# Performance work log

Measured on AMD Instinct MI355X. Metric: run time of the kernel, lower is better.

Reference implementation:

```python
import jax, jax.numpy as jnp
import numpy as np

M, K, N = 131072, 512, 512


def setup_inputs() -> dict:
    key = jax.random.key(0)
    k1, k2, k3, k4 = jax.random.split(key, 4)
    # Simulated int8 quantized values held in float32 (real kernel uses int8)
    x = jnp.round(jax.random.normal(k1, (M, K), dtype=jnp.float32) * 30.0)
    weight = jnp.round(jax.random.normal(k2, (N, K), dtype=jnp.float32) * 30.0)
    # per-token activation scale [M,1], per-output-channel weight scale [N]
    x_scale = jax.random.uniform(k3, (M, 1), dtype=jnp.float32, minval=1e-3, maxval=2e-2)
    weight_scale = jax.random.uniform(k4, (N,), dtype=jnp.float32, minval=1e-3, maxval=2e-2)
    return {"x": x, "x_scale": x_scale, "weight": weight, "weight_scale": weight_scale}


def reference(x, x_scale, weight, weight_scale):
    # gemm_a8w8(per_Token): out[m,n] = (sum_k x[m,k]*W[n,k]) * x_scale[m] * w_scale[n]
    acc = jnp.einsum('mk,nk->mn', x, weight)          # [M, N] int32-equivalent accum
    out = acc * x_scale * weight_scale[None, :]       # fused dequant scaling
    return out  # otype would be bf16 in the original; kept fp32 as reference baseline
```

## Files before the change

kernel.cpp:

```cpp
#include <hip/hip_runtime.h>
#include <hip/hip_bf16.h>
#include <stdint.h>

#define K_DIM 512
#define N_DIM 512
#define BM 64
#define CHUNK_K 64
#define CHUNK_FLOATS (BM * CHUNK_K)

typedef __bf16 bf16x8 __attribute__((ext_vector_type(8)));
typedef float floatx4 __attribute__((ext_vector_type(4)));

__device__ __forceinline__ bf16x8 cvt8(float4 a, float4 b) {
    bf16x8 r;
    r[0] = (__bf16)a.x; r[1] = (__bf16)a.y; r[2] = (__bf16)a.z; r[3] = (__bf16)a.w;
    r[4] = (__bf16)b.x; r[5] = (__bf16)b.y; r[6] = (__bf16)b.z; r[7] = (__bf16)b.w;
    return r;
}

__global__ __launch_bounds__(512) void wconv_kernel(const float* __restrict__ w,
                                                    __bf16* __restrict__ wf) {
    int t = blockIdx.x * 512 + threadIdx.x;
    int lane = t & 63, slot = t >> 6;
    int n = ((slot >> 4) << 4) + (lane & 15);
    int k = ((slot & 15) << 5) + ((lane >> 4) << 3);
    const float* src = w + (size_t)n * K_DIM + k;
    float4 f0 = *(const float4*)src;
    float4 f1 = *(const float4*)(src + 4);
    *(bf16x8*)(wf + (size_t)t * 8) = cvt8(f0, f1);
}

__device__ __forceinline__ void stage_chunk(const float* __restrict__ x,
                                            int rowBase, int kBase,
                                            float* ldsBuf, int wid, int lane) {
    #pragma unroll
    for (int i = 0; i < 2; ++i) {
        int sl = i * 8 + wid;
        int row = sl * 4 + (lane >> 4);
        int srcByte = ((lane & 15) << 4) ^ ((row & 7) << 4);
        const float* g = x + (size_t)(rowBase + row) * K_DIM + kBase + (srcByte >> 2);
        float* l = ldsBuf + sl * 1024 / 4;
        __builtin_amdgcn_global_load_lds(
            (const __attribute__((address_space(1))) void*)g,
            (__attribute__((address_space(3))) void*)l, 16, 0, 0);
    }
}

__device__ __forceinline__ bf16x8 read_afrag(const float* ldsBuf, int mg, int rt,
                                             int kcl, int lane) {
    int row = mg * 32 + rt * 16 + (lane & 15);
    int sw = (row & 7) << 4;
    int b0 = kcl * 128 + ((lane >> 4) << 5);
    const char* rb = (const char*)(ldsBuf + row * CHUNK_K);
    float4 fa = *(const float4*)(rb + (b0 ^ sw));
    float4 fb = *(const float4*)(rb + ((b0 + 16) ^ sw));
    return cvt8(fa, fb);
}

template <bool USE_WF>
__global__ __launch_bounds__(512, 2) void gemm_kernel(
    const float* __restrict__ x, const float* __restrict__ xscale,
    const __bf16* __restrict__ wf, const float* __restrict__ w,
    const float* __restrict__ wscale, float* __restrict__ out,
    int ntiles, int tilesPerBlock)
{
    __shared__ float lds[2 * CHUNK_FLOATS];
    const int t = threadIdx.x;
    const int lane = t & 63;
    const int wid = t >> 6;
    const int mg = wid >> 2;
    const int ng = wid & 3;
    const int laneR = lane & 15;

    const int tile0 = blockIdx.x * tilesPerBlock;
    if (tile0 >= ntiles) return;
    const int tileEnd = (tile0 + tilesPerBlock < ntiles) ? (tile0 + tilesPerBlock) : ntiles;
    const int nChunks = (tileEnd - tile0) * 8;

    floatx4 acc[2][8];
    bf16x8 wfr[8][2];

    stage_chunk(x, tile0 * BM, 0, &lds[0], wid, lane);

    for (int c = 0; c < nChunks; ++c) {
        const int tile = tile0 + (c >> 3);
        const int kk = c & 7;

        if (c > 0)
            asm volatile("s_waitcnt lgkmcnt(0)\n\ts_barrier" ::: "memory");

        #pragma unroll
        for (int nt = 0; nt < 8; ++nt) {
            int ntg = ng * 8 + nt;
            #pragma unroll
            for (int kcl = 0; kcl < 2; ++kcl) {
                int kcg = kk * 2 + kcl;
                if (USE_WF) {
                    wfr[nt][kcl] = *(const bf16x8*)(wf + (size_t)(((ntg << 4) + kcg) * 64 + lane) * 8);
                } else {
                    int n = (ntg << 4) + laneR;
                    const float* src = w + (size_t)n * K_DIM + (kcg << 5) + ((lane >> 4) << 3);
                    wfr[nt][kcl] = cvt8(*(const float4*)src, *(const float4*)(src + 4));
                }
            }
        }
        __builtin_amdgcn_sched_barrier(0);

        if (c + 1 < nChunks) {
            int cn = c + 1;
            stage_chunk(x, (tile0 + (cn >> 3)) * BM, (cn & 7) * CHUNK_K,
                        &lds[(cn & 1) * CHUNK_FLOATS], wid, lane);
            __builtin_amdgcn_sched_barrier(0);
            asm volatile("s_waitcnt vmcnt(2)\n\ts_barrier" ::: "memory");
        } else {
            asm volatile("s_waitcnt vmcnt(0)\n\ts_barrier" ::: "memory");
        }

        if (kk == 0) {
            #pragma unroll
            for (int i = 0; i < 2; ++i)
                #pragma unroll
                for (int j = 0; j < 8; ++j) acc[i][j] = (floatx4)0.f;
        }

        const float* cb = &lds[(c & 1) * CHUNK_FLOATS];
        #pragma unroll
        for (int kcl = 0; kcl < 2; ++kcl) {
            bf16x8 ax[2];
            #pragma unroll
            for (int rt = 0; rt < 2; ++rt)
                ax[rt] = read_afrag(cb, mg, rt, kcl, lane);
            #pragma unroll
            for (int nt = 0; nt < 8; ++nt)
                #pragma unroll
                for (int rt = 0; rt < 2; ++rt)
                    acc[rt][nt] = __builtin_amdgcn_mfma_f32_16x16x32_bf16(
                        wfr[nt][kcl], ax[rt], acc[rt][nt], 0, 0, 0);
        }

        if (kk == 7) {
            const int rowb = tile * BM;
            #pragma unroll
            for (int rt = 0; rt < 2; ++rt) {
                int m = rowb + mg * 32 + rt * 16 + laneR;
                float xs = xscale[m];
                #pragma unroll
                for (int nt = 0; nt < 8; ++nt) {
                    int nb = ng * 128 + (nt << 4) + ((lane >> 4) << 2);
                    float4 wsc = *(const float4*)(wscale + nb);
                    floatx4 a = acc[rt][nt];
                    float4 o;
                    o.x = a[0] * xs * wsc.x;
                    o.y = a[1] * xs * wsc.y;
                    o.z = a[2] * xs * wsc.z;
                    o.w = a[3] * xs * wsc.w;
                    *(float4*)(out + (size_t)m * N_DIM + nb) = o;
                }
            }
        }
    }
}

extern "C" void kernel_launch(void* const* d_in, const int* in_sizes, int n_in,
                              void* d_out, int out_size, void* d_ws, size_t ws_size,
                              hipStream_t stream) {
    const float* x      = (const float*)d_in[0];
    const float* xscale = (const float*)d_in[1];
    const float* w      = (const float*)d_in[2];
    const float* wscale = (const float*)d_in[3];
    float* out          = (float*)d_out;

    const int M = in_sizes[0] / K_DIM;
    const int ntiles = M / BM;
    const int nblocks = (ntiles < 256) ? ntiles : 256;
    const int tpb = (ntiles + nblocks - 1) / nblocks;

    if (ws_size >= (size_t)(N_DIM * K_DIM * sizeof(unsigned short))) {
        __bf16* wfp = (__bf16*)d_ws;
        wconv_kernel<<<dim3(64), dim3(512), 0, stream>>>(w, wfp);
        gemm_kernel<true><<<dim3(nblocks), dim3(512), 0, stream>>>(
            x, xscale, wfp, w, wscale, out, ntiles, tpb);
    } else {
        gemm_kernel<false><<<dim3(nblocks), dim3(512), 0, stream>>>(
            x, xscale, nullptr, w, wscale, out, ntiles, tpb);
    }
}
```

Measured before the change: 233.4 us.

## Use 1024-thread blocks with triple-buffered LDS and prefetched weight fragments

Doubles the block to 16 waves so each wave owns a 64-wide N slice, which halves the per-wave accumulators and weight fragments. The x staging ring grows from two to three LDS buffers and is issued two chunks ahead, and the next chunk's weight fragments are loaded into a second register set while the current chunk computes. The goal is to hide global load latency behind the MFMA work. In exchange there are more waves per block synchronising at each barrier, and the hand-tuned vmcnt counts must exactly match the number of outstanding loads.

```diff
diff --git a/kernel.cpp b/kernel.cpp
--- a/kernel.cpp
+++ b/kernel.cpp
@@ -7,6 +7,7 @@
 #define BM 64
 #define CHUNK_K 64
 #define CHUNK_FLOATS (BM * CHUNK_K)
+#define NBUF 3
 
 typedef __bf16 bf16x8 __attribute__((ext_vector_type(8)));
 typedef float floatx4 __attribute__((ext_vector_type(4)));
@@ -33,17 +34,13 @@
 __device__ __forceinline__ void stage_chunk(const float* __restrict__ x,
                                             int rowBase, int kBase,
                                             float* ldsBuf, int wid, int lane) {
-    #pragma unroll
-    for (int i = 0; i < 2; ++i) {
-        int sl = i * 8 + wid;
-        int row = sl * 4 + (lane >> 4);
-        int srcByte = ((lane & 15) << 4) ^ ((row & 7) << 4);
-        const float* g = x + (size_t)(rowBase + row) * K_DIM + kBase + (srcByte >> 2);
-        float* l = ldsBuf + sl * 1024 / 4;
-        __builtin_amdgcn_global_load_lds(
-            (const __attribute__((address_space(1))) void*)g,
-            (__attribute__((address_space(3))) void*)l, 16, 0, 0);
-    }
+    int row = wid * 4 + (lane >> 4);
+    int srcByte = ((lane & 15) << 4) ^ ((row & 7) << 4);
+    const float* g = x + (size_t)(rowBase + row) * K_DIM + kBase + (srcByte >> 2);
+    float* l = ldsBuf + wid * 256;
+    __builtin_amdgcn_global_load_lds(
+        (const __attribute__((address_space(1))) void*)g,
+        (__attribute__((address_space(3))) void*)l, 16, 0, 0);
 }
 
 __device__ __forceinline__ bf16x8 read_afrag(const float* ldsBuf, int mg, int rt,
@@ -58,106 +55,141 @@
 }
 
 template <bool USE_WF>
-__global__ __launch_bounds__(512, 2) void gemm_kernel(
+__device__ __forceinline__ void load_wfrag(bf16x8 (&dst)[4][2], int c,
+                                           const __bf16* __restrict__ wf,
+                                           const float* __restrict__ w,
+                                           int ng, int lane) {
+    int kk = c & 7;
+    #pragma unroll
+    for (int nt = 0; nt < 4; ++nt) {
+        int ntg = ng * 4 + nt;
+        #pragma unroll
+        for (int kcl = 0; kcl < 2; ++kcl) {
+            int kcg = kk * 2 + kcl;
+            if (USE_WF) {
+                dst[nt][kcl] = *(const bf16x8*)(wf + (size_t)(((ntg << 4) + kcg) * 64 + lane) * 8);
+            } else {
+                int n = (ntg << 4) + (lane & 15);
+                const float* s = w + (size_t)n * K_DIM + (kcg << 5) + ((lane >> 4) << 3);
+                dst[nt][kcl] = cvt8(*(const float4*)s, *(const float4*)(s + 4));
+            }
+        }
+    }
+}
+
+template <bool USE_WF>
+__device__ __forceinline__ void chunk_body(
+    int c, int nChunks, int ibR, int tile0,
+    const float* __restrict__ x, const float* __restrict__ xscale,
+    const __bf16* __restrict__ wf, const float* __restrict__ w,
+    const float* __restrict__ wscale, float* __restrict__ out,
+    float* lds, bf16x8 (&wfU)[4][2], bf16x8 (&wfF)[4][2], floatx4 (&acc)[2][4],
+    int wid, int lane, int mg, int ng)
+{
+    constexpr int WOPS = USE_WF ? 8 : 16;
+    const int laneR = lane & 15;
+
+    asm volatile("s_waitcnt lgkmcnt(0)\n\ts_barrier" ::: "memory");
+
+    {
+        int cn = (c + 1 < nChunks) ? c + 1 : nChunks - 1;
+        load_wfrag<USE_WF>(wfF, cn, wf, w, ng, lane);
+    }
+    __builtin_amdgcn_sched_barrier(0);
+
+    {
+        int cs = (c + 2 < nChunks) ? c + 2 : nChunks - 1;
+        int ibS = ibR + 2; if (ibS >= NBUF) ibS -= NBUF;
+        stage_chunk(x, (tile0 + (cs >> 3)) * BM, (cs & 7) * CHUNK_K,
+                    lds + ibS * CHUNK_FLOATS, wid, lane);
+    }
+    __builtin_amdgcn_sched_barrier(0);
+
+    if (c > 0 && (c & 7) == 0)
+        asm volatile("s_waitcnt vmcnt(%0)\n\ts_barrier" :: "i"(WOPS + 12) : "memory");
+    else
+        asm volatile("s_waitcnt vmcnt(%0)\n\ts_barrier" :: "i"(WOPS + 2) : "memory");
+
+    if ((c & 7) == 0) {
+        #pragma unroll
+        for (int i = 0; i < 2; ++i)
+            #pragma unroll
+            for (int j = 0; j < 4; ++j) acc[i][j] = (floatx4)0.f;
+    }
+
+    const float* cb = lds + ibR * CHUNK_FLOATS;
+    #pragma unroll
+    for (int kcl = 0; kcl < 2; ++kcl) {
+        bf16x8 ax[2];
+        #pragma unroll
+        for (int rt = 0; rt < 2; ++rt)
+            ax[rt] = read_afrag(cb, mg, rt, kcl, lane);
+        #pragma unroll
+        for (int nt = 0; nt < 4; ++nt)
+            #pragma unroll
+            for (int rt = 0; rt < 2; ++rt)
+                acc[rt][nt] = __builtin_amdgcn_mfma_f32_16x16x32_bf16(
+                    wfU[nt][kcl], ax[rt], acc[rt][nt], 0, 0, 0);
+    }
+
+    if ((c & 7) == 7) {
+        const int rowb = (tile0 + (c >> 3)) * BM;
+        #pragma unroll
+        for (int rt = 0; rt < 2; ++rt) {
+            int m = rowb + mg * 32 + rt * 16 + laneR;
+            float xs = xscale[m];
+            #pragma unroll
+            for (int nt = 0; nt < 4; ++nt) {
+                int nb = ng * 64 + (nt << 4) + ((lane >> 4) << 2);
+                float4 wsc = *(const float4*)(wscale + nb);
+                floatx4 a = acc[rt][nt];
+                float4 o;
+                o.x = a[0] * xs * wsc.x;
+                o.y = a[1] * xs * wsc.y;
+                o.z = a[2] * xs * wsc.z;
+                o.w = a[3] * xs * wsc.w;
+                *(float4*)(out + (size_t)m * N_DIM + nb) = o;
+            }
+        }
+    }
+}
+
+template <bool USE_WF>
+__global__ __launch_bounds__(1024) void gemm_kernel(
     const float* __restrict__ x, const float* __restrict__ xscale,
     const __bf16* __restrict__ wf, const float* __restrict__ w,
     const float* __restrict__ wscale, float* __restrict__ out,
     int ntiles, int tilesPerBlock)
 {
-    __shared__ float lds[2 * CHUNK_FLOATS];
+    __shared__ __align__(16) float lds[NBUF * CHUNK_FLOATS];
     const int t = threadIdx.x;
     const int lane = t & 63;
     const int wid = t >> 6;
-    const int mg = wid >> 2;
-    const int ng = wid & 3;
-    const int laneR = lane & 15;
+    const int mg = wid >> 3;
+    const int ng = wid & 7;
 
     const int tile0 = blockIdx.x * tilesPerBlock;
     if (tile0 >= ntiles) return;
     const int tileEnd = (tile0 + tilesPerBlock < ntiles) ? (tile0 + tilesPerBlock) : ntiles;
     const int nChunks = (tileEnd - tile0) * 8;
 
-    floatx4 acc[2][8];
-    bf16x8 wfr[8][2];
-
-    stage_chunk(x, tile0 * BM, 0, &lds[0], wid, lane);
-
-    for (int c = 0; c < nChunks; ++c) {
-        const int tile = tile0 + (c >> 3);
-        const int kk = c & 7;
-
-        if (c > 0)
-            asm volatile("s_waitcnt lgkmcnt(0)\n\ts_barrier" ::: "memory");
-
-        #pragma unroll
-        for (int nt = 0; nt < 8; ++nt) {
-            int ntg = ng * 8 + nt;
-            #pragma unroll
-            for (int kcl = 0; kcl < 2; ++kcl) {
-                int kcg = kk * 2 + kcl;
-                if (USE_WF) {
-                    wfr[nt][kcl] = *(const bf16x8*)(wf + (size_t)(((ntg << 4) + kcg) * 64 + lane) * 8);
-                } else {
-                    int n = (ntg << 4) + laneR;
-                    const float* src = w + (size_t)n * K_DIM + (kcg << 5) + ((lane >> 4) << 3);
-                    wfr[nt][kcl] = cvt8(*(const float4*)src, *(const float4*)(src + 4));
-                }
-            }
-        }
-        __builtin_amdgcn_sched_barrier(0);
-
-        if (c + 1 < nChunks) {
-            int cn = c + 1;
-            stage_chunk(x, (tile0 + (cn >> 3)) * BM, (cn & 7) * CHUNK_K,
-                        &lds[(cn & 1) * CHUNK_FLOATS], wid, lane);
-            __builtin_amdgcn_sched_barrier(0);
-            asm volatile("s_waitcnt vmcnt(2)\n\ts_barrier" ::: "memory");
-        } else {
-            asm volatile("s_waitcnt vmcnt(0)\n\ts_barrier" ::: "memory");
-        }
-
-        if (kk == 0) {
-            #pragma unroll
-            for (int i = 0; i < 2; ++i)
-                #pragma unroll
-                for (int j = 0; j < 8; ++j) acc[i][j] = (floatx4)0.f;
-        }
-
-        const float* cb = &lds[(c & 1) * CHUNK_FLOATS];
-        #pragma unroll
-        for (int kcl = 0; kcl < 2; ++kcl) {
-            bf16x8 ax[2];
-            #pragma unroll
-            for (int rt = 0; rt < 2; ++rt)
-                ax[rt] = read_afrag(cb, mg, rt, kcl, lane);
-            #pragma unroll
-            for (int nt = 0; nt < 8; ++nt)
-                #pragma unroll
-                for (int rt = 0; rt < 2; ++rt)
-                    acc[rt][nt] = __builtin_amdgcn_mfma_f32_16x16x32_bf16(
-                        wfr[nt][kcl], ax[rt], acc[rt][nt], 0, 0, 0);
-        }
-
-        if (kk == 7) {
-            const int rowb = tile * BM;
-            #pragma unroll
-            for (int rt = 0; rt < 2; ++rt) {
-                int m = rowb + mg * 32 + rt * 16 + laneR;
-                float xs = xscale[m];
-                #pragma unroll
-                for (int nt = 0; nt < 8; ++nt) {
-                    int nb = ng * 128 + (nt << 4) + ((lane >> 4) << 2);
-                    float4 wsc = *(const float4*)(wscale + nb);
-                    floatx4 a = acc[rt][nt];
-                    float4 o;
-                    o.x = a[0] * xs * wsc.x;
-                    o.y = a[1] * xs * wsc.y;
-                    o.z = a[2] * xs * wsc.z;
-                    o.w = a[3] * xs * wsc.w;
-                    *(float4*)(out + (size_t)m * N_DIM + nb) = o;
-                }
-            }
-        }
+    floatx4 acc[2][4];
+    bf16x8 wfrA[4][2], wfrB[4][2];
+
+    stage_chunk(x, tile0 * BM, 0, lds, wid, lane);
+    load_wfrag<USE_WF>(wfrA, 0, wf, w, ng, lane);
+    __builtin_amdgcn_sched_barrier(0);
+    stage_chunk(x, tile0 * BM, CHUNK_K, lds + CHUNK_FLOATS, wid, lane);
+    __builtin_amdgcn_sched_barrier(0);
+
+    int ibR = 0;
+    for (int c = 0; c < nChunks; c += 2) {
+        chunk_body<USE_WF>(c, nChunks, ibR, tile0, x, xscale, wf, w, wscale, out,
+                           lds, wfrA, wfrB, acc, wid, lane, mg, ng);
+        ibR = (ibR + 1 < NBUF) ? ibR + 1 : 0;
+        chunk_body<USE_WF>(c + 1, nChunks, ibR, tile0, x, xscale, wf, w, wscale, out,
+                           lds, wfrB, wfrA, acc, wid, lane, mg, ng);
+        ibR = (ibR + 1 < NBUF) ? ibR + 1 : 0;
     }
 }
 
@@ -178,10 +210,10 @@
     if (ws_size >= (size_t)(N_DIM * K_DIM * sizeof(unsigned short))) {
         __bf16* wfp = (__bf16*)d_ws;
         wconv_kernel<<<dim3(64), dim3(512), 0, stream>>>(w, wfp);
-        gemm_kernel<true><<<dim3(nblocks), dim3(512), 0, stream>>>(
+        gemm_kernel<true><<<dim3(nblocks), dim3(1024), 0, stream>>>(
             x, xscale, wfp, w, wscale, out, ntiles, tpb);
     } else {
-        gemm_kernel<false><<<dim3(nblocks), dim3(512), 0, stream>>>(
+        gemm_kernel<false><<<dim3(nblocks), dim3(1024), 0, stream>>>(
             x, xscale, nullptr, w, wscale, out, ntiles, tpb);
     }
 }
```

Measured after the change: 251.4 us. 7.7% more time.
